# Kernel tuning notes

Measured on AMD Instinct MI355X. Metric: run time of the kernel, lower is better.

The kernel has to match this reference:

```python
import jax, jax.numpy as jnp
import numpy as np

COST_CLASS, COST_BBOX, COST_GIOU = 1.0, 5.0, 2.0
NUM_FRAMES, Q_PER_FRAME, NUM_TGT, NUM_CLASSES = 36, 100, 20, 92
B = 64


def box_cxcywh_to_xyxy(b):
    cx, cy, w, h = b[..., 0], b[..., 1], b[..., 2], b[..., 3]
    return jnp.stack([cx - 0.5 * w, cy - 0.5 * h, cx + 0.5 * w, cy + 0.5 * h], axis=-1)


def pairwise_giou(b1, b2):
    # b1: [..., Q, 4], b2: [..., T, 4], xyxy -> giou [..., Q, T]
    area1 = (b1[..., 2] - b1[..., 0]) * (b1[..., 3] - b1[..., 1])
    area2 = (b2[..., 2] - b2[..., 0]) * (b2[..., 3] - b2[..., 1])
    lt = jnp.maximum(b1[..., :, None, :2], b2[..., None, :, :2])
    rb = jnp.minimum(b1[..., :, None, 2:], b2[..., None, :, 2:])
    wh = jnp.clip(rb - lt, 0.0)
    inter = wh[..., 0] * wh[..., 1]
    union = area1[..., :, None] + area2[..., None, :] - inter
    iou = inter / union
    lt_e = jnp.minimum(b1[..., :, None, :2], b2[..., None, :, :2])
    rb_e = jnp.maximum(b1[..., :, None, 2:], b2[..., None, :, 2:])
    wh_e = jnp.clip(rb_e - lt_e, 0.0)
    area_e = wh_e[..., 0] * wh_e[..., 1]
    return iou - (area_e - union) / area_e


def compute_cost(pred_logits, pred_boxes, tgt_labels, tgt_boxes):
    b = pred_logits.shape[0]
    prob = jax.nn.softmax(pred_logits.reshape(b, NUM_FRAMES, Q_PER_FRAME, -1), axis=-1)  # [B,F,Q,C]
    pb = pred_boxes.reshape(b, NUM_FRAMES, Q_PER_FRAME, 4)
    lab = jnp.transpose(tgt_labels, (1, 0, 2))            # [B,F,T]
    tb = jnp.transpose(tgt_boxes, (1, 0, 2, 3))           # [B,F,T,4]
    onehot = jax.nn.one_hot(lab, prob.shape[-1], dtype=prob.dtype)  # [B,F,T,C]
    cost_class = -jnp.einsum('bfqc,bftc->bfqt', prob, onehot)
    cost_bbox = jnp.abs(pb[:, :, :, None, :] - tb[:, :, None, :, :]).sum(-1)  # L1 cdist
    giou = pairwise_giou(box_cxcywh_to_xyxy(pb), box_cxcywh_to_xyxy(tb))
    return COST_CLASS * cost_class + COST_BBOX * cost_bbox - COST_GIOU * giou


def auction_assign(cost):
    # cost [Q, T]; returns obj_of [T]: query index assigned to each target.
    # eps-optimal auction algorithm (replaces scipy linear_sum_assignment).
    Q, T = cost.shape
    benefit = -cost.T  # [T, Q]
    spread = jnp.max(benefit) - jnp.min(benefit) + 1e-6
    eps = spread / 1000.0
    neg_inf = jnp.asarray(-1e30, cost.dtype)

    def cond(s):
        _, _, obj_of, it = s
        return jnp.logical_and(jnp.any(obj_of < 0), it < 20000)

    def body(s):
        price, owner, obj_of, it = s
        unassigned = obj_of < 0                       # [T]
        vals = benefit - price[None, :]               # [T, Q]
        top2v, top2i = jax.lax.top_k(vals, 2)
        best_obj = top2i[:, 0]                        # [T]
        bid = price[best_obj] + (top2v[:, 0] - top2v[:, 1]) + eps
        bid = jnp.where(unassigned, bid, neg_inf)
        best_bid = jnp.full((Q,), neg_inf, cost.dtype).at[best_obj].max(bid)
        pids = jnp.arange(T, dtype=jnp.int32)
        win = unassigned & (bid >= best_bid[best_obj])
        winner = jnp.full((Q,), T, jnp.int32).at[best_obj].min(jnp.where(win, pids, T))
        has_bid = winner < T
        # evict previous owners of objects that received a bid
        evict = jnp.where(has_bid & (owner >= 0), owner, T)
        obj_of = obj_of.at[evict].set(-1, mode='drop')
        qids = jnp.arange(Q, dtype=jnp.int32)
        obj_of = obj_of.at[jnp.where(has_bid, winner, T)].set(jnp.where(has_bid, qids, -1), mode='drop')
        price = jnp.where(has_bid, best_bid, price)
        owner = jnp.where(has_bid, winner, owner)
        return price, owner, obj_of, it + 1

    init = (jnp.zeros((Q,), cost.dtype), jnp.full((Q,), -1, jnp.int32),
            jnp.full((T,), -1, jnp.int32), jnp.int32(0))
    _, _, obj_of, _ = jax.lax.while_loop(cond, body, init)
    return obj_of


def setup_inputs() -> dict:
    key = jax.random.key(0)
    k1, k2, k3, k4 = jax.random.split(key, 4)
    pred_logits = jax.random.normal(k1, (B, NUM_FRAMES * Q_PER_FRAME, NUM_CLASSES), jnp.float32)
    pred_boxes = jax.random.uniform(k2, (B, NUM_FRAMES * Q_PER_FRAME, 4), jnp.float32)
    tgt_labels = jax.random.randint(k3, (NUM_FRAMES, B, NUM_TGT), 0, NUM_CLASSES, jnp.int32)
    tgt_boxes = jax.random.uniform(k4, (NUM_FRAMES, B, NUM_TGT, 4), jnp.float32)
    return {'pred_logits': pred_logits, 'pred_boxes': pred_boxes,
            'tgt_labels': tgt_labels, 'tgt_boxes': tgt_boxes}


def reference(pred_logits, pred_boxes, tgt_labels, tgt_boxes):
    cost = compute_cost(pred_logits, pred_boxes, tgt_labels, tgt_boxes)  # [B,F,Q,T]
    b, f, q, t = cost.shape
    obj_of = jax.vmap(auction_assign)(cost.reshape(b * f, q, t))  # [BF, T]
    order = jnp.argsort(obj_of, axis=-1)  # scipy returns rows ascending
    pred_idx = jnp.take_along_axis(obj_of, order, axis=-1).reshape(b, f, t)
    tgt_idx = order.astype(jnp.int32).reshape(b, f, t)
    return cost, pred_idx, tgt_idx
```

## Files before the change

### kernel.cpp

```cpp
#include <hip/hip_runtime.h>

#define NF 36
#define QN 100
#define TN 20
#define CN 92
#define NB 64
#define BSTR 104

struct T2 { float v0, v1, p0; int i0; };

__global__ __launch_bounds__(64) void matcher_kernel(
    const float* __restrict__ logits,
    const float* __restrict__ pboxes,
    const int*   __restrict__ tlabels,
    const float* __restrict__ tboxes,
    float* __restrict__ out_cost,
    float* __restrict__ out_pred,
    float* __restrict__ out_tgt)
{
    const int bf = blockIdx.x;
    const int b  = bf / NF;
    const int f  = bf % NF;
    const int lane = threadIdx.x;

    __shared__ __align__(16) float ben[TN][BSTR];
    __shared__ __align__(16) float price[BSTR];
    __shared__ int   objl[TN];
    __shared__ int   slab[TN];
    __shared__ float tbr[TN][4];
    __shared__ float tbx[TN][4];
    __shared__ float tarea[TN];

    if (lane < TN) {
        const int base = (f * NB + b) * TN + lane;
        slab[lane] = tlabels[base];
        const float* tb = tboxes + (size_t)base * 4;
        float cx = tb[0], cy = tb[1], w = tb[2], h = tb[3];
        tbr[lane][0] = cx; tbr[lane][1] = cy; tbr[lane][2] = w; tbr[lane][3] = h;
        float x1 = cx - 0.5f * w, y1 = cy - 0.5f * h;
        float x2 = cx + 0.5f * w, y2 = cy + 0.5f * h;
        tbx[lane][0] = x1; tbx[lane][1] = y1; tbx[lane][2] = x2; tbx[lane][3] = y2;
        tarea[lane] = (x2 - x1) * (y2 - y1);
    }
    __syncthreads();

    float mn = INFINITY, mx = -INFINITY;
    for (int p = 0; p < 2; ++p) {
        const int q = lane + 64 * p;
        if (q < QN) {
            const size_t row = (size_t)b * (NF * QN) + (size_t)f * QN + q;
            const float* L = logits + row * CN;
            const float4* L4 = reinterpret_cast<const float4*>(L);
            float4 r[23];
            #pragma unroll
            for (int i = 0; i < 23; ++i) r[i] = L4[i];
            float m = -INFINITY;
            #pragma unroll
            for (int i = 0; i < 23; ++i) {
                float4 v = r[i];
                m = fmaxf(m, v.x); m = fmaxf(m, v.y); m = fmaxf(m, v.z); m = fmaxf(m, v.w);
            }
            float s = 0.f;
            #pragma unroll
            for (int i = 0; i < 23; ++i) {
                float4 v = r[i];
                s += expf(v.x - m); s += expf(v.y - m); s += expf(v.z - m); s += expf(v.w - m);
            }

            float4 pbv = reinterpret_cast<const float4*>(pboxes)[row];
            float cx = pbv.x, cy = pbv.y, w = pbv.z, h = pbv.w;
            float px1 = cx - 0.5f * w, py1 = cy - 0.5f * h;
            float px2 = cx + 0.5f * w, py2 = cy + 0.5f * h;
            float a1 = (px2 - px1) * (py2 - py1);

            for (int t = 0; t < TN; ++t) {
                float pc = expf(L[slab[t]] - m) / s;
                float cb = fabsf(cx - tbr[t][0]) + fabsf(cy - tbr[t][1]);
                cb = cb + fabsf(w - tbr[t][2]);
                cb = cb + fabsf(h - tbr[t][3]);
                float ltx = fmaxf(px1, tbx[t][0]), lty = fmaxf(py1, tbx[t][1]);
                float rbx = fminf(px2, tbx[t][2]), rby = fminf(py2, tbx[t][3]);
                float wx = fmaxf(rbx - ltx, 0.f), wy = fmaxf(rby - lty, 0.f);
                float inter = wx * wy;
                float uni = a1 + tarea[t] - inter;
                float iou = inter / uni;
                float ex1 = fminf(px1, tbx[t][0]), ey1 = fminf(py1, tbx[t][1]);
                float ex2 = fmaxf(px2, tbx[t][2]), ey2 = fmaxf(py2, tbx[t][3]);
                float ew = fmaxf(ex2 - ex1, 0.f), eh = fmaxf(ey2 - ey1, 0.f);
                float ae = ew * eh;
                float giou = iou - (ae - uni) / ae;
                float cost = (-pc) + 5.0f * cb - 2.0f * giou;
                ben[t][q] = -cost;
                mn = fminf(mn, cost);
                mx = fmaxf(mx, cost);
            }
        }
    }

    for (int i = lane; i < BSTR; i += 64) price[i] = 0.f;
    if (lane < TN) {
        ben[lane][100] = -INFINITY; ben[lane][101] = -INFINITY;
        ben[lane][102] = -INFINITY; ben[lane][103] = -INFINITY;
    }
    __syncthreads();

    #pragma unroll
    for (int off = 32; off > 0; off >>= 1) {
        mn = fminf(mn, __shfl_xor(mn, off, 64));
        mx = fmaxf(mx, __shfl_xor(mx, off, 64));
    }
    const float eps = (((-mn) - (-mx)) + 1e-6f) / 1000.0f;

    {
        float4* dst = reinterpret_cast<float4*>(out_cost + (size_t)bf * (QN * TN));
        for (int i = lane; i < (QN * TN) / 4; i += 64) {
            int k = i * 4;
            int q = k / TN, t0 = k - q * TN;
            float4 v;
            v.x = -ben[t0 + 0][q]; v.y = -ben[t0 + 1][q];
            v.z = -ben[t0 + 2][q]; v.w = -ben[t0 + 3][q];
            dst[i] = v;
        }
    }

    const int myt = lane / 3;
    const int jj  = lane - myt * 3;
    const int q0  = (jj == 0) ? 0 : (jj == 1 ? 36 : 68);
    const bool is_leader = (lane < 60) && (jj == 0);
    float4 br[9];
    {
        const int tt = (lane < 60) ? myt : 0;
        const float4* rp = reinterpret_cast<const float4*>(&ben[tt][q0]);
        #pragma unroll
        for (int k = 0; k < 9; ++k) br[k] = rp[k];
    }
    int myobj = -1;

    auto step4 = [&](T2& X, int fi) {
        float4 pv = *reinterpret_cast<const float4*>(&price[q0 + 4 * fi]);
        float4 bv = br[fi];
        { float v = bv.x - pv.x; bool c = v > X.v0; X.v1 = c ? X.v0 : fmaxf(X.v1, v); X.i0 = c ? (q0+4*fi+0) : X.i0; X.p0 = c ? pv.x : X.p0; X.v0 = c ? v : X.v0; }
        { float v = bv.y - pv.y; bool c = v > X.v0; X.v1 = c ? X.v0 : fmaxf(X.v1, v); X.i0 = c ? (q0+4*fi+1) : X.i0; X.p0 = c ? pv.y : X.p0; X.v0 = c ? v : X.v0; }
        { float v = bv.z - pv.z; bool c = v > X.v0; X.v1 = c ? X.v0 : fmaxf(X.v1, v); X.i0 = c ? (q0+4*fi+2) : X.i0; X.p0 = c ? pv.z : X.p0; X.v0 = c ? v : X.v0; }
        { float v = bv.w - pv.w; bool c = v > X.v0; X.v1 = c ? X.v0 : fmaxf(X.v1, v); X.i0 = c ? (q0+4*fi+3) : X.i0; X.p0 = c ? pv.w : X.p0; X.v0 = c ? v : X.v0; }
    };
    auto mergeT = [&](T2& L, const T2& R) {
        if (R.v0 > L.v0) { L.v1 = fmaxf(L.v0, R.v1); L.v0 = R.v0; L.i0 = R.i0; L.p0 = R.p0; }
        else             { L.v1 = fmaxf(R.v0, L.v1); }
    };

    for (int it = 0; it < 20000; ++it) {
        const bool active = is_leader && (myobj < 0);
        unsigned long long U = __ballot(active);
        if (U == 0ull) break;

        T2 A{-INFINITY, -INFINITY, 0.f, q0};
        T2 Bc{-INFINITY, -INFINITY, 0.f, q0 + 12};
        T2 Cc{-INFINITY, -INFINITY, 0.f, q0 + 24};
        step4(A, 0);  step4(A, 1);  step4(A, 2);
        step4(Bc, 3); step4(Bc, 4); step4(Bc, 5);
        step4(Cc, 6); step4(Cc, 7);
        if (jj != 1) step4(Cc, 8);
        mergeT(A, Bc); mergeT(A, Cc);

        {
            T2 R1{__shfl_down(A.v0, 1), __shfl_down(A.v1, 1), __shfl_down(A.p0, 1), __shfl_down(A.i0, 1)};
            T2 R2{__shfl_down(A.v0, 2), __shfl_down(A.v1, 2), __shfl_down(A.p0, 2), __shfl_down(A.i0, 2)};
            mergeT(A, R1); mergeT(A, R2);
        }
        float mybid = A.p0 + (A.v0 - A.v1) + eps;
        float bb_ = active ? mybid : -INFINITY;
        int   bq  = A.i0;

        bool lose = false, evicted = false;
        if (__popcll(U) == 1) {
            int src = (int)__builtin_ctzll(U);
            int sq = __shfl(bq, src);
            evicted = (myobj == sq);
        } else {
            #pragma unroll
            for (int t2 = 0; t2 < TN; ++t2) {
                float sb = __shfl(bb_, 3 * t2);
                int   sq = __shfl(bq, 3 * t2);
                bool a2 = (sb != -INFINITY);
                lose    = lose    || (a2 && sq == bq   && (sb > bb_ || (sb == bb_ && t2 < myt)));
                evicted = evicted || (a2 && sq == myobj);
            }
        }
        if (active && !lose) { price[bq] = mybid; myobj = bq; }
        else if (is_leader && evicted && myobj >= 0) myobj = -1;
        __syncthreads();
    }
    __syncthreads();
    if (is_leader) objl[myt] = myobj;
    __syncthreads();

    if (lane < TN) {
        int v = objl[lane];
        int r = 0;
        for (int u = 0; u < TN; ++u) {
            int w = objl[u];
            r += (w < v) || (w == v && u < lane);
        }
        out_pred[(size_t)bf * TN + r] = (float)v;
        out_tgt[(size_t)bf * TN + r]  = (float)lane;
    }
}

extern "C" void kernel_launch(void* const* d_in, const int* in_sizes, int n_in,
                              void* d_out, int out_size, void* d_ws, size_t ws_size,
                              hipStream_t stream) {
    const float* logits  = (const float*)d_in[0];
    const float* pboxes  = (const float*)d_in[1];
    const int*   tlabels = (const int*)d_in[2];
    const float* tboxes  = (const float*)d_in[3];

    float* out = (float*)d_out;
    float* out_cost = out;
    float* out_pred = out + (size_t)NB * NF * QN * TN;
    float* out_tgt  = out_pred + (size_t)NB * NF * TN;

    hipLaunchKernelGGL(matcher_kernel, dim3(NB * NF), dim3(64), 0, stream,
                       logits, pboxes, tlabels, tboxes, out_cost, out_pred, out_tgt);
}
```

Baseline: 185.9 us.

## Adaptively split the auction bid scan across lanes by active bidder count

The auction loop used a fixed 3 lanes per target, each holding its benefit row in registers. It now assigns 64/popc lanes (rounded to a power of two) to each active bidder, reads benefits from shared memory, and reduces with an xor butterfly. Conflict resolution now loops only over the active bidders instead of all 20 targets. The goal is to shorten the serial tail of iterations where only a few targets are still bidding, at the cost of more shared-memory reads and extra branching per iteration.

```diff
diff --git a/kernel.cpp b/kernel.cpp
--- a/kernel.cpp
+++ b/kernel.cpp
@@ -5,9 +5,86 @@
 #define TN 20
 #define CN 92
 #define NB 64
-#define BSTR 104
+#define BSTR 136
 
 struct T2 { float v0, v1, p0; int i0; };
+
+__device__ __forceinline__ void mergeT(T2& L, const T2& R) {
+    if (R.v0 > L.v0) { L.v1 = fmaxf(L.v0, R.v1); L.v0 = R.v0; L.i0 = R.i0; L.p0 = R.p0; }
+    else             { L.v1 = fmaxf(R.v0, L.v1); }
+}
+
+__device__ __forceinline__ void elemT(T2& X, float bv, float pv, int q) {
+    float v = bv - pv;
+    bool c = v > X.v0;
+    X.v1 = c ? X.v0 : fmaxf(X.v1, v);
+    X.i0 = c ? q : X.i0;
+    X.p0 = c ? pv : X.p0;
+    X.v0 = c ? v : X.v0;
+}
+
+template<int G>
+__device__ __forceinline__ void scan_deliver(const float (*ben)[BSTR], const float* price,
+                                             unsigned long long U, int lane, float eps,
+                                             float& mybid, int& bq) {
+    constexpr int E = 128 / G;
+    constexpr int S = E / 4;
+    const int k = lane / G;
+    const int r = lane % G;
+    unsigned long long u = U;
+    #pragma unroll 1
+    for (int i = 0; i < k && u; ++i) u &= (u - 1);
+    const int t = u ? (int)__builtin_ctzll(u) : 0;
+    const float* rb = ben[t];
+    const int qb = r * E;
+
+    T2 A{-INFINITY, -INFINITY, 0.f, qb};
+    if constexpr (S == 1) {
+        float4 bv = *(const float4*)(rb + qb);
+        float4 pv = *(const float4*)(price + qb);
+        elemT(A, bv.x, pv.x, qb);     elemT(A, bv.y, pv.y, qb + 1);
+        elemT(A, bv.z, pv.z, qb + 2); elemT(A, bv.w, pv.w, qb + 3);
+    } else {
+        constexpr int SH = S / 2;
+        T2 B{-INFINITY, -INFINITY, 0.f, qb + SH * 4};
+        #pragma unroll
+        for (int fi = 0; fi < SH; ++fi) {
+            int q = qb + fi * 4;
+            float4 bv = *(const float4*)(rb + q);
+            float4 pv = *(const float4*)(price + q);
+            elemT(A, bv.x, pv.x, q);     elemT(A, bv.y, pv.y, q + 1);
+            elemT(A, bv.z, pv.z, q + 2); elemT(A, bv.w, pv.w, q + 3);
+        }
+        #pragma unroll
+        for (int fi = SH; fi < S; ++fi) {
+            int q = qb + fi * 4;
+            float4 bv = *(const float4*)(rb + q);
+            float4 pv = *(const float4*)(price + q);
+            elemT(B, bv.x, pv.x, q);     elemT(B, bv.y, pv.y, q + 1);
+            elemT(B, bv.z, pv.z, q + 2); elemT(B, bv.w, pv.w, q + 3);
+        }
+        mergeT(A, B);
+    }
+    #pragma unroll
+    for (int off = 1; off < G; off <<= 1) {
+        T2 R;
+        R.v0 = __shfl_xor(A.v0, off);
+        R.v1 = __shfl_xor(A.v1, off);
+        R.p0 = __shfl_xor(A.p0, off);
+        R.i0 = __shfl_xor(A.i0, off);
+        bool hi = (lane & off) != 0;
+        T2 Lh, Rh;
+        Lh.v0 = hi ? R.v0 : A.v0; Lh.v1 = hi ? R.v1 : A.v1; Lh.p0 = hi ? R.p0 : A.p0; Lh.i0 = hi ? R.i0 : A.i0;
+        Rh.v0 = hi ? A.v0 : R.v0; Rh.v1 = hi ? A.v1 : R.v1; Rh.p0 = hi ? A.p0 : R.p0; Rh.i0 = hi ? A.i0 : R.i0;
+        mergeT(Lh, Rh);
+        A = Lh;
+    }
+    float gbid = A.p0 + (A.v0 - A.v1) + eps;
+    int slot = (int)__popcll(U & ((1ull << lane) - 1));
+    int src = (slot * G) & 63;
+    mybid = __shfl(gbid, src);
+    bq    = __shfl(A.i0, src);
+}
 
 __global__ __launch_bounds__(64) void matcher_kernel(
     const float* __restrict__ logits,
@@ -98,9 +175,10 @@
     }
 
     for (int i = lane; i < BSTR; i += 64) price[i] = 0.f;
-    if (lane < TN) {
-        ben[lane][100] = -INFINITY; ben[lane][101] = -INFINITY;
-        ben[lane][102] = -INFINITY; ben[lane][103] = -INFINITY;
+    for (int i = lane; i < TN * (BSTR - QN); i += 64) {
+        int t = i / (BSTR - QN);
+        int qq = QN + (i - t * (BSTR - QN));
+        ben[t][qq] = -INFINITY;
     }
     __syncthreads();
 
@@ -122,77 +200,44 @@
             dst[i] = v;
         }
     }
-
-    const int myt = lane / 3;
-    const int jj  = lane - myt * 3;
-    const int q0  = (jj == 0) ? 0 : (jj == 1 ? 36 : 68);
-    const bool is_leader = (lane < 60) && (jj == 0);
-    float4 br[9];
-    {
-        const int tt = (lane < 60) ? myt : 0;
-        const float4* rp = reinterpret_cast<const float4*>(&ben[tt][q0]);
-        #pragma unroll
-        for (int k = 0; k < 9; ++k) br[k] = rp[k];
-    }
+    __syncthreads();
+
+    const float (*benc)[BSTR] = (const float (*)[BSTR])ben;
     int myobj = -1;
-
-    auto step4 = [&](T2& X, int fi) {
-        float4 pv = *reinterpret_cast<const float4*>(&price[q0 + 4 * fi]);
-        float4 bv = br[fi];
-        { float v = bv.x - pv.x; bool c = v > X.v0; X.v1 = c ? X.v0 : fmaxf(X.v1, v); X.i0 = c ? (q0+4*fi+0) : X.i0; X.p0 = c ? pv.x : X.p0; X.v0 = c ? v : X.v0; }
-        { float v = bv.y - pv.y; bool c = v > X.v0; X.v1 = c ? X.v0 : fmaxf(X.v1, v); X.i0 = c ? (q0+4*fi+1) : X.i0; X.p0 = c ? pv.y : X.p0; X.v0 = c ? v : X.v0; }
-        { float v = bv.z - pv.z; bool c = v > X.v0; X.v1 = c ? X.v0 : fmaxf(X.v1, v); X.i0 = c ? (q0+4*fi+2) : X.i0; X.p0 = c ? pv.z : X.p0; X.v0 = c ? v : X.v0; }
-        { float v = bv.w - pv.w; bool c = v > X.v0; X.v1 = c ? X.v0 : fmaxf(X.v1, v); X.i0 = c ? (q0+4*fi+3) : X.i0; X.p0 = c ? pv.w : X.p0; X.v0 = c ? v : X.v0; }
-    };
-    auto mergeT = [&](T2& L, const T2& R) {
-        if (R.v0 > L.v0) { L.v1 = fmaxf(L.v0, R.v1); L.v0 = R.v0; L.i0 = R.i0; L.p0 = R.p0; }
-        else             { L.v1 = fmaxf(R.v0, L.v1); }
-    };
-
     for (int it = 0; it < 20000; ++it) {
-        const bool active = is_leader && (myobj < 0);
+        const bool active = (lane < TN) && (myobj < 0);
         unsigned long long U = __ballot(active);
         if (U == 0ull) break;
-
-        T2 A{-INFINITY, -INFINITY, 0.f, q0};
-        T2 Bc{-INFINITY, -INFINITY, 0.f, q0 + 12};
-        T2 Cc{-INFINITY, -INFINITY, 0.f, q0 + 24};
-        step4(A, 0);  step4(A, 1);  step4(A, 2);
-        step4(Bc, 3); step4(Bc, 4); step4(Bc, 5);
-        step4(Cc, 6); step4(Cc, 7);
-        if (jj != 1) step4(Cc, 8);
-        mergeT(A, Bc); mergeT(A, Cc);
-
-        {
-            T2 R1{__shfl_down(A.v0, 1), __shfl_down(A.v1, 1), __shfl_down(A.p0, 1), __shfl_down(A.i0, 1)};
-            T2 R2{__shfl_down(A.v0, 2), __shfl_down(A.v1, 2), __shfl_down(A.p0, 2), __shfl_down(A.i0, 2)};
-            mergeT(A, R1); mergeT(A, R2);
-        }
-        float mybid = A.p0 + (A.v0 - A.v1) + eps;
-        float bb_ = active ? mybid : -INFINITY;
-        int   bq  = A.i0;
+        const int popc = (int)__popcll(U);
+
+        float mybid; int bq;
+        if      (popc <= 2)  scan_deliver<32>(benc, price, U, lane, eps, mybid, bq);
+        else if (popc <= 4)  scan_deliver<16>(benc, price, U, lane, eps, mybid, bq);
+        else if (popc <= 8)  scan_deliver<8 >(benc, price, U, lane, eps, mybid, bq);
+        else if (popc <= 16) scan_deliver<4 >(benc, price, U, lane, eps, mybid, bq);
+        else                 scan_deliver<2 >(benc, price, U, lane, eps, mybid, bq);
 
         bool lose = false, evicted = false;
-        if (__popcll(U) == 1) {
+        if (popc == 1) {
             int src = (int)__builtin_ctzll(U);
             int sq = __shfl(bq, src);
             evicted = (myobj == sq);
         } else {
-            #pragma unroll
-            for (int t2 = 0; t2 < TN; ++t2) {
-                float sb = __shfl(bb_, 3 * t2);
-                int   sq = __shfl(bq, 3 * t2);
-                bool a2 = (sb != -INFINITY);
-                lose    = lose    || (a2 && sq == bq   && (sb > bb_ || (sb == bb_ && t2 < myt)));
-                evicted = evicted || (a2 && sq == myobj);
+            float sendb = active ? mybid : -INFINITY;
+            unsigned long long u = U;
+            while (u) {
+                int t2 = (int)__builtin_ctzll(u); u &= (u - 1);
+                float sb = __shfl(sendb, t2);
+                int   sq = __shfl(bq, t2);
+                lose    = lose    || (sq == bq   && (sb > mybid || (sb == mybid && t2 < lane)));
+                evicted = evicted || (sq == myobj);
             }
         }
         if (active && !lose) { price[bq] = mybid; myobj = bq; }
-        else if (is_leader && evicted && myobj >= 0) myobj = -1;
+        else if (evicted && myobj >= 0) myobj = -1;
         __syncthreads();
     }
-    __syncthreads();
-    if (is_leader) objl[myt] = myobj;
+    if (lane < TN) objl[lane] = myobj;
     __syncthreads();
 
     if (lane < TN) {
```

Result: slower. 193.2 us (+4.0%).
